# Performance work log

Hardware: AMD Instinct MI355X
Metric: run time of the kernel (lower is better)

## Reference

```python
import jax, jax.numpy as jnp
import numpy as np

L, B, H, P = 2048, 32, 128, 256  # seq len, batch, feature dim, state dim


def setup_inputs() -> dict:
    key = jax.random.key(0)
    ks = jax.random.split(key, 9)
    log_min, log_max = np.log(0.001), np.log(0.1)
    return {
        "input_sequences": jax.random.normal(ks[0], (L, B, H), dtype=jnp.float32),
        # -Lambda.real of a HiPPO block diag is positive; emulate with small positive values
        "log_Lambda_real": jnp.log(0.5 + jax.random.uniform(ks[1], (P,), dtype=jnp.float32)),
        "Lambda_imag": jax.random.normal(ks[2], (P,), dtype=jnp.float32) * 3.0,
        "B_tilde_r": jax.random.normal(ks[3], (P, H), dtype=jnp.float32) * (0.5 / np.sqrt(H)),
        "B_tilde_i": jax.random.normal(ks[4], (P, H), dtype=jnp.float32) * (0.5 / np.sqrt(H)),
        "C_tilde_r": jax.random.normal(ks[5], (H, P), dtype=jnp.float32) * (0.5 / np.sqrt(P)),
        "C_tilde_i": jax.random.normal(ks[6], (H, P), dtype=jnp.float32) * (0.5 / np.sqrt(P)),
        "D": jax.random.normal(ks[7], (H,), dtype=jnp.float32),
        "log_Delta": log_min + (log_max - log_min) * jax.random.uniform(ks[8], (P,), dtype=jnp.float32),
    }


def reference(input_sequences, log_Lambda_real, Lambda_imag, B_tilde_r, B_tilde_i,
              C_tilde_r, C_tilde_i, D, log_Delta):
    l = input_sequences.shape[0]
    u = input_sequences.astype(jnp.complex64)  # (L,B,H)
    lam = (-jnp.exp(log_Lambda_real) + 1j * Lambda_imag).astype(jnp.complex64)  # (P,)
    log_Lambda_bar = lam * jnp.exp(log_Delta).astype(jnp.complex64)  # scale_factor=1.0
    # kernel[t, p] = exp(log_Lambda_bar[p] * (L-1-t))  -> (L,P)
    steps = jnp.arange(l - 1, -1, -1, dtype=jnp.float32).astype(jnp.complex64)
    kernel = jnp.exp(steps[:, None] * log_Lambda_bar[None, :])
    B_tilde = (B_tilde_r + 1j * B_tilde_i).astype(jnp.complex64)  # (P,H)
    B_bar = ((kernel[-2] - 1.0) / lam)[:, None] * B_tilde  # (P,H)
    Bu = jnp.einsum('nm,lbm->lbn', B_bar, u)  # (L,B,P)
    # FFT convolution: flipped kernel is exp(log_Lambda_bar * t)
    kff = jnp.fft.fft(kernel[::-1], n=2 * l, axis=0)[:, None, :]  # (2L,1,P)
    buff = jnp.fft.fft(Bu, n=2 * l, axis=0)  # (2L,B,P)
    o = jnp.fft.ifft(kff * buff, axis=0)[:l]  # (L,B,P)
    xs = jnp.einsum('hn,lbn->lbh', (C_tilde_r + 1j * C_tilde_i).astype(jnp.complex64), o)
    xs = xs + (D * input_sequences).astype(jnp.complex64)
    return jnp.real(xs)
```

## Files before the change

kernel.cpp:

```cpp
#include <hip/hip_runtime.h>
#include <math.h>

#define SL 2048
#define NB 32
#define NH 128
#define NP 256
#define NP2 512

typedef short bf16x8 __attribute__((ext_vector_type(8)));
typedef float f32x4  __attribute__((ext_vector_type(4)));

static __device__ __forceinline__ unsigned short f2bf(float x) {
    unsigned u = __float_as_uint(x);
    return (unsigned short)((u + 0x7fffu + ((u >> 16) & 1u)) >> 16);
}
static __device__ __forceinline__ float bf2f(unsigned short h) {
    return __uint_as_float(((unsigned)h) << 16);
}
static __device__ __forceinline__ void discretize(
    const float* __restrict__ logLr, const float* __restrict__ Lim,
    const float* __restrict__ logDt, int p, float& wr, float& wi)
{
    const float Lr = expf(logLr[p]);
    const float dt = expf(logDt[p]);
    const float ew = expf(-Lr * dt);
    const float ang = Lim[p] * dt;
    wr = ew * cosf(ang); wi = ew * sinf(ang);
}

__global__ __launch_bounds__(256) void k0(
    const float* __restrict__ logLr, const float* __restrict__ Lim,
    const float* __restrict__ logDt,
    const float* __restrict__ Br, const float* __restrict__ Bi,
    const float* __restrict__ Cr, const float* __restrict__ Ci,
    unsigned short* __restrict__ Bhat, unsigned short* __restrict__ ChatF)
{
    const int tid = blockIdx.x * 256 + threadIdx.x;
    const int p = tid >> 7, h = tid & 127;
    float wr, wi; discretize(logLr, Lim, logDt, p, wr, wi);
    const float Lr = expf(logLr[p]), li = Lim[p];
    const float nr = wr - 1.0f, ni = wi;
    const float den = Lr * Lr + li * li;
    const float fr = (-nr * Lr + ni * li) / den;
    const float fi = (-ni * Lr - nr * li) / den;
    const float br = Br[p * NH + h], bi = Bi[p * NH + h];
    Bhat[(size_t)(2 * p)     * NH + h] = f2bf(fr * br - fi * bi);
    Bhat[(size_t)(2 * p + 1) * NH + h] = f2bf(fr * bi + fi * br);
    const int col0 = 2 * p, col1 = 2 * p + 1;
    ChatF[((size_t)(col0 >> 5) << 12) + (h << 5) + (col0 & 31)] = f2bf(Cr[h * NP + p]);
    ChatF[((size_t)(col1 >> 5) << 12) + (h << 5) + (col1 & 31)] = f2bf(-Ci[h * NP + p]);
}

__global__ __launch_bounds__(256, 2) void gA(
    const float* __restrict__ u, const unsigned short* __restrict__ Bhat,
    const float* __restrict__ logLr, const float* __restrict__ Lim,
    const float* __restrict__ logDt,
    unsigned short* __restrict__ bu, float2* __restrict__ part)
{
    __shared__ unsigned short us[32][136];
    __shared__ unsigned xs[32 * 257];

    const int seg = blockIdx.x;
    const int b   = blockIdx.y;
    const int tid = threadIdx.x;
    const int wave = tid >> 6, lane = tid & 63;
    const int q = lane >> 4, c = lane & 15;
    const int pbase = wave * 128;

    bf16x8 A[4][8];
    #pragma unroll
    for (int kk = 0; kk < 4; ++kk)
        #pragma unroll
        for (int mt = 0; mt < 8; ++mt)
            A[kk][mt] = *(const bf16x8*)(Bhat + (size_t)(pbase + 16 * mt + c) * NH
                                              + kk * 32 + 8 * q);

    float wr, wi; discretize(logLr, Lim, logDt, tid, wr, wi);
    float W32r = wr, W32i = wi;
    #pragma unroll
    for (int t = 0; t < 5; ++t) { const float r = W32r * W32r - W32i * W32i;
                                  W32i = 2.f * W32r * W32i; W32r = r; }

    float2 pa = make_float2(0.f, 0.f);

    for (int t = 0; t < 4; ++t) {
        const int l0 = seg * 128 + t * 32;
        __syncthreads();
        {
            const int lrow = tid >> 3;
            const int hcol = (tid & 7) * 16;
            const float* up = u + (size_t)(l0 + lrow) * (NB * NH) + b * NH + hcol;
            float4 a = *(const float4*)(up + 0);
            float4 d = *(const float4*)(up + 4);
            float4 e = *(const float4*)(up + 8);
            float4 g = *(const float4*)(up + 12);
            uint4 w0, w1;
            w0.x = (unsigned)f2bf(a.x) | ((unsigned)f2bf(a.y) << 16);
            w0.y = (unsigned)f2bf(a.z) | ((unsigned)f2bf(a.w) << 16);
            w0.z = (unsigned)f2bf(d.x) | ((unsigned)f2bf(d.y) << 16);
            w0.w = (unsigned)f2bf(d.z) | ((unsigned)f2bf(d.w) << 16);
            w1.x = (unsigned)f2bf(e.x) | ((unsigned)f2bf(e.y) << 16);
            w1.y = (unsigned)f2bf(e.z) | ((unsigned)f2bf(e.w) << 16);
            w1.z = (unsigned)f2bf(g.x) | ((unsigned)f2bf(g.y) << 16);
            w1.w = (unsigned)f2bf(g.z) | ((unsigned)f2bf(g.w) << 16);
            *(uint4*)&us[lrow][hcol + 0] = w0;
            *(uint4*)&us[lrow][hcol + 8] = w1;
        }
        __syncthreads();

        f32x4 acc[8][2];
        #pragma unroll
        for (int mt = 0; mt < 8; ++mt)
            #pragma unroll
            for (int nt = 0; nt < 2; ++nt) acc[mt][nt] = (f32x4){0.f, 0.f, 0.f, 0.f};

        #pragma unroll
        for (int kk = 0; kk < 4; ++kk) {
            bf16x8 bfr[2];
            #pragma unroll
            for (int nt = 0; nt < 2; ++nt)
                bfr[nt] = *(const bf16x8*)&us[16 * nt + c][kk * 32 + 8 * q];
            #pragma unroll
            for (int mt = 0; mt < 8; ++mt)
                #pragma unroll
                for (int nt = 0; nt < 2; ++nt)
                    acc[mt][nt] = __builtin_amdgcn_mfma_f32_16x16x32_bf16(
                        A[kk][mt], bfr[nt], acc[mt][nt], 0, 0, 0);
        }

        #pragma unroll
        for (int mt = 0; mt < 8; ++mt)
            #pragma unroll
            for (int nt = 0; nt < 2; ++nt) {
                const int rw = 16 * nt + c;
                const int pp = pbase + 16 * mt + 4 * q;
                ushort4 st;
                st.x = f2bf(acc[mt][nt][0]); st.y = f2bf(acc[mt][nt][1]);
                st.z = f2bf(acc[mt][nt][2]); st.w = f2bf(acc[mt][nt][3]);
                *(ushort4*)(bu + ((size_t)(b * SL + l0 + rw)) * NP2 + pp) = st;
                const int col = (pp >> 1);
                xs[rw * 257 + col]     = (unsigned)st.x | ((unsigned)st.y << 16);
                xs[rw * 257 + col + 1] = (unsigned)st.z | ((unsigned)st.w << 16);
            }
        __syncthreads();

        {
            float sr = 0.f, si = 0.f;
            unsigned va[8], vb[8];
            #pragma unroll
            for (int j = 0; j < 8; ++j) va[j] = xs[j * 257 + tid];
            #pragma unroll
            for (int k8 = 0; k8 < 4; ++k8) {
                if (k8 < 3) {
                    #pragma unroll
                    for (int j = 0; j < 8; ++j) vb[j] = xs[((k8 + 1) * 8 + j) * 257 + tid];
                }
                #pragma unroll
                for (int j = 0; j < 8; ++j) {
                    const float xr = bf2f((unsigned short)(va[j] & 0xffffu));
                    const float xi = bf2f((unsigned short)(va[j] >> 16));
                    const float tr = wr * sr - wi * si + xr;
                    const float ti = wr * si + wi * sr + xi;
                    sr = tr; si = ti;
                }
                #pragma unroll
                for (int j = 0; j < 8; ++j) va[j] = vb[j];
            }
            if ((t & 1) == 0) {
                pa = make_float2(sr, si);
            } else {
                const float cr2 = W32r * pa.x - W32i * pa.y + sr;
                const float ci2 = W32r * pa.y + W32i * pa.x + si;
                part[((size_t)b * 32 + 2 * seg + (t >> 1)) * NP + tid] =
                    make_float2(cr2, ci2);
            }
        }
    }
}

__global__ __launch_bounds__(256) void s2(
    const float2* __restrict__ part, const float* __restrict__ logLr,
    const float* __restrict__ Lim, const float* __restrict__ logDt,
    float2* __restrict__ C)
{
    const int b = blockIdx.x, p = threadIdx.x;
    float wr, wi; discretize(logLr, Lim, logDt, p, wr, wi);
    float Wr = wr, Wi = wi;
    #pragma unroll
    for (int t = 0; t < 6; ++t) { const float r = Wr * Wr - Wi * Wi; Wi = 2.f * Wr * Wi; Wr = r; }
    float sr = 0.f, si = 0.f;
    for (int m = 0; m < 32; ++m) {
        C[(size_t)(b * 32 + m) * NP + p] = make_float2(sr, si);
        const float2 v = part[(size_t)(b * 32 + m) * NP + p];
        const float tr = Wr * sr - Wi * si + v.x;
        const float ti = Wr * si + Wi * sr + v.y;
        sr = tr; si = ti;
    }
}

__global__ __launch_bounds__(256, 4) void gB(
    const unsigned* __restrict__ bu32, const unsigned short* __restrict__ ChatF,
    const float* __restrict__ logLr, const float* __restrict__ Lim,
    const float* __restrict__ logDt, const float2* __restrict__ C,
    const float* __restrict__ Dv, const float* __restrict__ u,
    float* __restrict__ out)
{
    __shared__ char   osb[32768];
    __shared__ float2 carr[2][3 * 128];

    const int m = blockIdx.x, b = blockIdx.y;
    const int tid = threadIdx.x;
    const int w = tid >> 6, lane = tid & 63;
    const int q = lane >> 4, c = lane & 15;
    const int wm = w >> 1, wn = w & 1;
    const int hbase = wm * 64;
    const int lbase = m * 64 + wn * 32;

    f32x4 acc[4][2];
    #pragma unroll
    for (int mt = 0; mt < 4; ++mt)
        #pragma unroll
        for (int nt = 0; nt < 2; ++nt) acc[mt][nt] = (f32x4){0.f, 0.f, 0.f, 0.f};

    #pragma unroll 1
    for (int half = 0; half < 2; ++half) {
        const int pc0 = half * 128 + lane * 2;

        float wr[2], wi[2];
        #pragma unroll
        for (int e = 0; e < 2; ++e) discretize(logLr, Lim, logDt, pc0 + e, wr[e], wi[e]);

        float Wr[2], Wi[2];
        #pragma unroll
        for (int e = 0; e < 2; ++e) { Wr[e] = wr[e]; Wi[e] = wi[e]; }
        #pragma unroll
        for (int t = 0; t < 4; ++t)
            #pragma unroll
            for (int e = 0; e < 2; ++e) {
                const float r = Wr[e] * Wr[e] - Wi[e] * Wi[e];
                Wi[e] = 2.f * Wr[e] * Wi[e]; Wr[e] = r;
            }

        const unsigned* base = bu32 + ((size_t)(b * SL + m * 64 + w * 16)) * NP
                                    + half * 128 + lane * 2;
        uint2 va[16];
        #pragma unroll
        for (int k = 0; k < 16; ++k) va[k] = *(const uint2*)(base + (size_t)k * NP);

        float sr[2] = {0.f, 0.f}, si[2] = {0.f, 0.f};
        #pragma unroll
        for (int k = 0; k < 16; ++k) {
            unsigned vv[2] = { va[k].x, va[k].y };
            #pragma unroll
            for (int e = 0; e < 2; ++e) {
                const float xr = bf2f((unsigned short)(vv[e] & 0xffffu));
                const float xi = bf2f((unsigned short)(vv[e] >> 16));
                const float tr = wr[e] * sr[e] - wi[e] * si[e] + xr;
                const float ti = wr[e] * si[e] + wi[e] * sr[e] + xi;
                sr[e] = tr; si[e] = ti;
            }
        }
        if (w < 3) {
            #pragma unroll
            for (int e = 0; e < 2; ++e)
                carr[half][w * 128 + lane * 2 + e] = make_float2(sr[e], si[e]);
        }

        float Er[2], Ei[2];
        #pragma unroll
        for (int e = 0; e < 2; ++e) {
            const float2 E = C[((size_t)(b * 32 + m)) * NP + pc0 + e];
            Er[e] = E.x; Ei[e] = E.y;
        }

        __syncthreads();

        #pragma unroll
        for (int j = 0; j < 3; ++j) if (j < w)
            #pragma unroll
            for (int e = 0; e < 2; ++e) {
                const float2 v = carr[half][j * 128 + lane * 2 + e];
                const float tr = Wr[e] * Er[e] - Wi[e] * Ei[e] + v.x;
                const float ti = Wr[e] * Ei[e] + Wi[e] * Er[e] + v.y;
                Er[e] = tr; Ei[e] = ti;
            }

        #pragma unroll
        for (int e = 0; e < 2; ++e) { sr[e] = Er[e]; si[e] = Ei[e]; }
        #pragma unroll
        for (int k = 0; k < 16; ++k) {
            unsigned vv[2] = { va[k].x, va[k].y };
            unsigned ov[2];
            #pragma unroll
            for (int e = 0; e < 2; ++e) {
                const float xr = bf2f((unsigned short)(vv[e] & 0xffffu));
                const float xi = bf2f((unsigned short)(vv[e] >> 16));
                const float tr = wr[e] * sr[e] - wi[e] * si[e] + xr;
                const float ti = wr[e] * si[e] + wi[e] * sr[e] + xi;
                sr[e] = tr; si[e] = ti;
                ov[e] = (unsigned)f2bf(tr) | ((unsigned)f2bf(ti) << 16);
            }
            const int row = w * 16 + k;
            const unsigned byte = (((unsigned)row << 9) + ((unsigned)lane << 3))
                                  ^ (((unsigned)(row & 7)) << 4);
            uint2 st = { ov[0], ov[1] };
            *(uint2*)(osb + byte) = st;
        }
        __syncthreads();

        #pragma unroll 4
        for (int kl = 0; kl < 8; ++kl) {
            const int kk = half * 8 + kl;
            bf16x8 af[4];
            #pragma unroll
            for (int mt = 0; mt < 4; ++mt)
                af[mt] = *(const bf16x8*)(ChatF + ((size_t)kk << 12)
                                          + ((hbase + (mt << 4) + c) << 5) + (q << 3));
            bf16x8 bfr[2];
            #pragma unroll
            for (int nt = 0; nt < 2; ++nt) {
                const int r = wn * 32 + 16 * nt + c;
                const unsigned byte = (((unsigned)r << 9) + ((unsigned)kl << 6)
                                       + ((unsigned)q << 4))
                                      ^ (((unsigned)(c & 7)) << 4);
                bfr[nt] = *(const bf16x8*)(osb + byte);
            }
            #pragma unroll
            for (int mt = 0; mt < 4; ++mt)
                #pragma unroll
                for (int nt = 0; nt < 2; ++nt)
                    acc[mt][nt] = __builtin_amdgcn_mfma_f32_16x16x32_bf16(
                        af[mt], bfr[nt], acc[mt][nt], 0, 0, 0);
        }
        if (half == 0) __syncthreads();
    }

    #pragma unroll
    for (int mt = 0; mt < 4; ++mt) {
        const int h4 = hbase + 16 * mt + 4 * q;
        const float4 dd = *(const float4*)(Dv + h4);
        #pragma unroll
        for (int nt = 0; nt < 2; ++nt) {
            const int l = lbase + 16 * nt + c;
            const size_t off = ((size_t)l * NB + b) * NH + h4;
            const float4 uu = *(const float4*)(u + off);
            float4 ov;
            ov.x = acc[mt][nt][0] + dd.x * uu.x;
            ov.y = acc[mt][nt][1] + dd.y * uu.y;
            ov.z = acc[mt][nt][2] + dd.z * uu.z;
            ov.w = acc[mt][nt][3] + dd.w * uu.w;
            *(float4*)(out + off) = ov;
        }
    }
}

extern "C" void kernel_launch(void* const* d_in, const int* in_sizes, int n_in,
                              void* d_out, int out_size, void* d_ws, size_t ws_size,
                              hipStream_t stream)
{
    const float* u     = (const float*)d_in[0];
    const float* logLr = (const float*)d_in[1];
    const float* Lim   = (const float*)d_in[2];
    const float* Btr   = (const float*)d_in[3];
    const float* Bti   = (const float*)d_in[4];
    const float* Ctr   = (const float*)d_in[5];
    const float* Cti   = (const float*)d_in[6];
    const float* Dv    = (const float*)d_in[7];
    const float* logDt = (const float*)d_in[8];
    float* out = (float*)d_out;

    char* ws = (char*)d_ws;
    unsigned short* bu   = (unsigned short*)ws;
    float2*         part = (float2*)(ws + 67108864);
    float2*         Cst  = (float2*)(ws + 69206016);
    unsigned short* Bhat = (unsigned short*)(ws + 71303168);
    unsigned short* Chat = (unsigned short*)(ws + 71434240);

    k0<<<dim3((NP * NH) / 256), 256, 0, stream>>>(logLr, Lim, logDt,
                                                  Btr, Bti, Ctr, Cti, Bhat, Chat);
    gA<<<dim3(16, NB), 256, 0, stream>>>(u, Bhat, logLr, Lim, logDt, bu, part);
    s2<<<dim3(NB), 256, 0, stream>>>(part, logLr, Lim, logDt, Cst);
    gB<<<dim3(SL / 64, NB), 256, 0, stream>>>((const unsigned*)bu, Chat, logLr, Lim,
                                              logDt, Cst, Dv, u, out);
}
```

Baseline: 176.2 us.

## Halve gB chunk to 32 timesteps and rescan 64 chunk carries in place

gA now writes one partial state per 32-step chunk instead of combining pairs into 64-step chunks. s2 scans 64 chunks per batch and overwrites the partials in place with entry states, which removes the separate carry buffer. gB processes 32-step tiles with 4 waves each owning 32 h-rows, half the shared memory, and 8 blocks per CU, doubling the grid. This shortens the per-block serial recurrence and raises occupancy, at the cost of a longer serial scan in s2, less MFMA reuse per block, and more repeated Chat loads.

```diff
diff --git a/kernel.cpp b/kernel.cpp
--- a/kernel.cpp
+++ b/kernel.cpp
@@ -76,12 +76,6 @@
                                               + kk * 32 + 8 * q);
 
     float wr, wi; discretize(logLr, Lim, logDt, tid, wr, wi);
-    float W32r = wr, W32i = wi;
-    #pragma unroll
-    for (int t = 0; t < 5; ++t) { const float r = W32r * W32r - W32i * W32i;
-                                  W32i = 2.f * W32r * W32i; W32r = r; }
-
-    float2 pa = make_float2(0.f, 0.f);
 
     for (int t = 0; t < 4; ++t) {
         const int l0 = seg * 128 + t * 32;
@@ -166,59 +160,51 @@
                 #pragma unroll
                 for (int j = 0; j < 8; ++j) va[j] = vb[j];
             }
-            if ((t & 1) == 0) {
-                pa = make_float2(sr, si);
-            } else {
-                const float cr2 = W32r * pa.x - W32i * pa.y + sr;
-                const float ci2 = W32r * pa.y + W32i * pa.x + si;
-                part[((size_t)b * 32 + 2 * seg + (t >> 1)) * NP + tid] =
-                    make_float2(cr2, ci2);
-            }
+            part[((size_t)b * 64 + seg * 4 + t) * NP + tid] = make_float2(sr, si);
         }
     }
 }
 
 __global__ __launch_bounds__(256) void s2(
-    const float2* __restrict__ part, const float* __restrict__ logLr,
-    const float* __restrict__ Lim, const float* __restrict__ logDt,
-    float2* __restrict__ C)
+    float2* __restrict__ part, const float* __restrict__ logLr,
+    const float* __restrict__ Lim, const float* __restrict__ logDt)
 {
     const int b = blockIdx.x, p = threadIdx.x;
     float wr, wi; discretize(logLr, Lim, logDt, p, wr, wi);
     float Wr = wr, Wi = wi;
     #pragma unroll
-    for (int t = 0; t < 6; ++t) { const float r = Wr * Wr - Wi * Wi; Wi = 2.f * Wr * Wi; Wr = r; }
+    for (int t = 0; t < 5; ++t) { const float r = Wr * Wr - Wi * Wi; Wi = 2.f * Wr * Wi; Wr = r; }
     float sr = 0.f, si = 0.f;
-    for (int m = 0; m < 32; ++m) {
-        C[(size_t)(b * 32 + m) * NP + p] = make_float2(sr, si);
-        const float2 v = part[(size_t)(b * 32 + m) * NP + p];
+    for (int m = 0; m < 64; ++m) {
+        const size_t idx = (size_t)(b * 64 + m) * NP + p;
+        const float2 v = part[idx];
+        part[idx] = make_float2(sr, si);
         const float tr = Wr * sr - Wi * si + v.x;
         const float ti = Wr * si + Wi * sr + v.y;
         sr = tr; si = ti;
     }
 }
 
-__global__ __launch_bounds__(256, 4) void gB(
+__global__ __launch_bounds__(256, 8) void gB(
     const unsigned* __restrict__ bu32, const unsigned short* __restrict__ ChatF,
     const float* __restrict__ logLr, const float* __restrict__ Lim,
-    const float* __restrict__ logDt, const float2* __restrict__ C,
+    const float* __restrict__ logDt, const float2* __restrict__ Ent,
     const float* __restrict__ Dv, const float* __restrict__ u,
     float* __restrict__ out)
 {
-    __shared__ char   osb[32768];
-    __shared__ float2 carr[2][3 * 128];
+    __shared__ char   osb[16384];
+    __shared__ float2 carr[3 * 128];
 
     const int m = blockIdx.x, b = blockIdx.y;
     const int tid = threadIdx.x;
     const int w = tid >> 6, lane = tid & 63;
     const int q = lane >> 4, c = lane & 15;
-    const int wm = w >> 1, wn = w & 1;
-    const int hbase = wm * 64;
-    const int lbase = m * 64 + wn * 32;
-
-    f32x4 acc[4][2];
+    const int hbase = w * 32;
+    const int lbase = m * 32;
+
+    f32x4 acc[2][2];
     #pragma unroll
-    for (int mt = 0; mt < 4; ++mt)
+    for (int mt = 0; mt < 2; ++mt)
         #pragma unroll
         for (int nt = 0; nt < 2; ++nt) acc[mt][nt] = (f32x4){0.f, 0.f, 0.f, 0.f};
 
@@ -234,22 +220,22 @@
         #pragma unroll
         for (int e = 0; e < 2; ++e) { Wr[e] = wr[e]; Wi[e] = wi[e]; }
         #pragma unroll
-        for (int t = 0; t < 4; ++t)
+        for (int t = 0; t < 3; ++t)
             #pragma unroll
             for (int e = 0; e < 2; ++e) {
                 const float r = Wr[e] * Wr[e] - Wi[e] * Wi[e];
                 Wi[e] = 2.f * Wr[e] * Wi[e]; Wr[e] = r;
             }
 
-        const unsigned* base = bu32 + ((size_t)(b * SL + m * 64 + w * 16)) * NP
+        const unsigned* base = bu32 + ((size_t)(b * SL + m * 32 + w * 8)) * NP
                                     + half * 128 + lane * 2;
-        uint2 va[16];
-        #pragma unroll
-        for (int k = 0; k < 16; ++k) va[k] = *(const uint2*)(base + (size_t)k * NP);
+        uint2 va[8];
+        #pragma unroll
+        for (int k = 0; k < 8; ++k) va[k] = *(const uint2*)(base + (size_t)k * NP);
 
         float sr[2] = {0.f, 0.f}, si[2] = {0.f, 0.f};
         #pragma unroll
-        for (int k = 0; k < 16; ++k) {
+        for (int k = 0; k < 8; ++k) {
             unsigned vv[2] = { va[k].x, va[k].y };
             #pragma unroll
             for (int e = 0; e < 2; ++e) {
@@ -263,13 +249,13 @@
         if (w < 3) {
             #pragma unroll
             for (int e = 0; e < 2; ++e)
-                carr[half][w * 128 + lane * 2 + e] = make_float2(sr[e], si[e]);
+                carr[w * 128 + lane * 2 + e] = make_float2(sr[e], si[e]);
         }
 
         float Er[2], Ei[2];
         #pragma unroll
         for (int e = 0; e < 2; ++e) {
-            const float2 E = C[((size_t)(b * 32 + m)) * NP + pc0 + e];
+            const float2 E = Ent[((size_t)(b * 64 + m)) * NP + pc0 + e];
             Er[e] = E.x; Ei[e] = E.y;
         }
 
@@ -279,7 +265,7 @@
         for (int j = 0; j < 3; ++j) if (j < w)
             #pragma unroll
             for (int e = 0; e < 2; ++e) {
-                const float2 v = carr[half][j * 128 + lane * 2 + e];
+                const float2 v = carr[j * 128 + lane * 2 + e];
                 const float tr = Wr[e] * Er[e] - Wi[e] * Ei[e] + v.x;
                 const float ti = Wr[e] * Ei[e] + Wi[e] * Er[e] + v.y;
                 Er[e] = tr; Ei[e] = ti;
@@ -288,7 +274,7 @@
         #pragma unroll
         for (int e = 0; e < 2; ++e) { sr[e] = Er[e]; si[e] = Ei[e]; }
         #pragma unroll
-        for (int k = 0; k < 16; ++k) {
+        for (int k = 0; k < 8; ++k) {
             unsigned vv[2] = { va[k].x, va[k].y };
             unsigned ov[2];
             #pragma unroll
@@ -300,7 +286,7 @@
                 sr[e] = tr; si[e] = ti;
                 ov[e] = (unsigned)f2bf(tr) | ((unsigned)f2bf(ti) << 16);
             }
-            const int row = w * 16 + k;
+            const int row = w * 8 + k;
             const unsigned byte = (((unsigned)row << 9) + ((unsigned)lane << 3))
                                   ^ (((unsigned)(row & 7)) << 4);
             uint2 st = { ov[0], ov[1] };
@@ -311,22 +297,22 @@
         #pragma unroll 4
         for (int kl = 0; kl < 8; ++kl) {
             const int kk = half * 8 + kl;
-            bf16x8 af[4];
-            #pragma unroll
-            for (int mt = 0; mt < 4; ++mt)
+            bf16x8 af[2];
+            #pragma unroll
+            for (int mt = 0; mt < 2; ++mt)
                 af[mt] = *(const bf16x8*)(ChatF + ((size_t)kk << 12)
                                           + ((hbase + (mt << 4) + c) << 5) + (q << 3));
             bf16x8 bfr[2];
             #pragma unroll
             for (int nt = 0; nt < 2; ++nt) {
-                const int r = wn * 32 + 16 * nt + c;
+                const int r = 16 * nt + c;
                 const unsigned byte = (((unsigned)r << 9) + ((unsigned)kl << 6)
                                        + ((unsigned)q << 4))
                                       ^ (((unsigned)(c & 7)) << 4);
                 bfr[nt] = *(const bf16x8*)(osb + byte);
             }
             #pragma unroll
-            for (int mt = 0; mt < 4; ++mt)
+            for (int mt = 0; mt < 2; ++mt)
                 #pragma unroll
                 for (int nt = 0; nt < 2; ++nt)
                     acc[mt][nt] = __builtin_amdgcn_mfma_f32_16x16x32_bf16(
@@ -336,7 +322,7 @@
     }
 
     #pragma unroll
-    for (int mt = 0; mt < 4; ++mt) {
+    for (int mt = 0; mt < 2; ++mt) {
         const int h4 = hbase + 16 * mt + 4 * q;
         const float4 dd = *(const float4*)(Dv + h4);
         #pragma unroll
@@ -372,14 +358,13 @@
     char* ws = (char*)d_ws;
     unsigned short* bu   = (unsigned short*)ws;
     float2*         part = (float2*)(ws + 67108864);
-    float2*         Cst  = (float2*)(ws + 69206016);
     unsigned short* Bhat = (unsigned short*)(ws + 71303168);
     unsigned short* Chat = (unsigned short*)(ws + 71434240);
 
     k0<<<dim3((NP * NH) / 256), 256, 0, stream>>>(logLr, Lim, logDt,
                                                   Btr, Bti, Ctr, Cti, Bhat, Chat);
     gA<<<dim3(16, NB), 256, 0, stream>>>(u, Bhat, logLr, Lim, logDt, bu, part);
-    s2<<<dim3(NB), 256, 0, stream>>>(part, logLr, Lim, logDt, Cst);
-    gB<<<dim3(SL / 64, NB), 256, 0, stream>>>((const unsigned*)bu, Chat, logLr, Lim,
-                                              logDt, Cst, Dv, u, out);
-}
+    s2<<<dim3(NB), 256, 0, stream>>>(part, logLr, Lim, logDt);
+    gB<<<dim3(SL / 32, NB), 256, 0, stream>>>((const unsigned*)bu, Chat, logLr, Lim,
+                                              logDt, part, Dv, u, out);
+}
```

Result: slower. 205.6 us (+16.7%).
